# Optimization experiments

Hardware: AMD Instinct MI355X
Metric: run time of the kernel (lower is better)

## Reference

```python
import jax, jax.numpy as jnp
import numpy as np

V, D, H, HD, L, T, B = 65, 384, 6, 64, 6, 256, 64
EPS = 1e-3  # keras LayerNormalization default epsilon


def setup_inputs() -> dict:
    key = jax.random.key(0)
    ks = jax.random.split(key, 12)
    s = 0.02
    n = lambda k, shp: jax.random.normal(k, shp, dtype=jnp.float32) * s
    return {
        "idx": jax.random.randint(ks[0], (B, T), 0, V),
        "tok_emb": n(ks[1], (V, D)),
        "pos_emb": n(ks[2], (T, D)),
        "Wq": n(ks[3], (L, H, D, HD)),
        "Wk": n(ks[4], (L, H, D, HD)),
        "Wv": n(ks[5], (L, H, D, HD)),
        "Wproj": n(ks[6], (L, D, D)),
        "bproj": jnp.zeros((L, D), jnp.float32),
        "W1": n(ks[7], (L, D, 4 * D)),
        "b1": jnp.zeros((L, 4 * D), jnp.float32),
        "W2": n(ks[8], (L, 4 * D, D)),
        "b2": jnp.zeros((L, D), jnp.float32),
        "ln1_g": jnp.ones((L, D), jnp.float32),
        "ln1_b": jnp.zeros((L, D), jnp.float32),
        "ln2_g": jnp.ones((L, D), jnp.float32),
        "ln2_b": jnp.zeros((L, D), jnp.float32),
        "lnf_g": jnp.ones((D,), jnp.float32),
        "lnf_b": jnp.zeros((D,), jnp.float32),
        "Whead": n(ks[9], (D, V)),
        "bhead": jnp.zeros((V,), jnp.float32),
    }


def _ln(x, g, b):
    m = jnp.mean(x, axis=-1, keepdims=True)
    v = jnp.mean(jnp.square(x - m), axis=-1, keepdims=True)
    return (x - m) * jax.lax.rsqrt(v + EPS) * g + b


def reference(idx, tok_emb, pos_emb, Wq, Wk, Wv, Wproj, bproj, W1, b1, W2, b2,
              ln1_g, ln1_b, ln2_g, ln2_b, lnf_g, lnf_b, Whead, bhead):
    Bn, Tn = idx.shape
    x = tok_emb[idx] + pos_emb[:Tn]  # [B,T,D]
    mask = jnp.tril(jnp.ones((Tn, Tn), dtype=bool))
    scale = jnp.float32(D) ** -0.5  # NOTE: original scales by full C=n_embd, not head_size
    for l in range(L):
        h = _ln(x, ln1_g[l], ln1_b[l])
        q = jnp.einsum('btd,hdk->bhtk', h, Wq[l])
        k = jnp.einsum('btd,hdk->bhtk', h, Wk[l])
        v = jnp.einsum('btd,hdk->bhtk', h, Wv[l])
        wei = jnp.einsum('bhtk,bhsk->bhts', q, k) * scale
        wei = jnp.where(mask, wei, -jnp.inf)
        wei = jax.nn.softmax(wei, axis=-1)
        att = jnp.einsum('bhts,bhsk->bhtk', wei, v)
        att = att.transpose(0, 2, 1, 3).reshape(Bn, Tn, D)  # concat heads
        x = x + att @ Wproj[l] + bproj[l]
        h2 = _ln(x, ln2_g[l], ln2_b[l])
        x = x + jax.nn.relu(h2 @ W1[l] + b1[l]) @ W2[l] + b2[l]
    x = _ln(x, lnf_g, lnf_b)
    return x @ Whead + bhead  # logits [B,T,V]
```

## Files before the change

### kernel.cpp

```cpp
#include <hip/hip_runtime.h>
#include <hip/hip_bf16.h>

#define B_  64
#define T_  256
#define D_  384
#define H_  6
#define HD_ 64
#define L_  6
#define V_  65
#define BT  (B_*T_)

typedef __hip_bfloat16 bf16;
typedef unsigned short u16;
typedef short s16;
typedef __attribute__((ext_vector_type(8))) short bf16x8;
typedef __attribute__((ext_vector_type(4))) float f32x4;

#define OFF_QKV   0
#define OFF_PROJ  442368
#define OFF_W1T   589824
#define OFF_W2T   1179648
#define OFF_BPROJ 1769472
#define OFF_B1    1769856
#define OFF_B2    1771392
#define OFF_LN1G  1771776
#define OFF_LN1B  1772160
#define OFF_LN2G  1772544
#define OFF_LN2B  1772928
#define WBUF_E    1773312
#define HOFF_WHT  0
#define HOFF_BH   24960
#define HOFF_LNFG 25088
#define HOFF_LNFB 25472
#define HBUF_E    25856

__device__ __forceinline__ float u2f(u16 u) {
  union { unsigned i; float f; } c; c.i = ((unsigned)u) << 16; return c.f;
}
__device__ __forceinline__ bf16 f2b(float x) { return __float2bfloat16(x); }
__device__ __forceinline__ float b2f(bf16 x) { return __bfloat162float(x); }
__device__ __forceinline__ u16 f2u(float x) { bf16 h = f2b(x); return *(u16*)&h; }

__device__ __forceinline__ float pload(const void* p, size_t i, bool f32w) {
  return f32w ? ((const float*)p)[i] : u2f(((const u16*)p)[i]);
}

__device__ __forceinline__ void swz(int gid, int ntc, int mtiles,
                                    int& nt, int& mblk) {
  if ((mtiles & 7) == 0) {
    int per = ntc << 3;
    int g   = gid / per;
    int rem = gid - g * per;
    nt   = rem >> 3;
    mblk = (g << 3) + (rem & 7);
  } else {
    nt   = gid / mtiles;
    mblk = gid - nt * mtiles;
  }
}

__global__ __launch_bounds__(256) void detect_kernel(
    const void* p1,  const void* p2,  const void* p3,  const void* p4,
    const void* p5,  const void* p6,  const void* p7,  const void* p8,
    const void* p9,  const void* p10, const void* p11, const void* p12,
    const void* p13, const void* p14, const void* p15, const void* p16,
    const void* p17, const void* p18, const void* p19,
    const int* __restrict__ idx, unsigned* flags)
{
  const void* ps[20] = {nullptr, p1, p2, p3, p4, p5, p6, p7, p8, p9, p10,
                        p11, p12, p13, p14, p15, p16, p17, p18, p19};
  const int esz[20] = {16384, 24960, 98304, 884736, 884736, 884736, 884736,
                       2304, 3538944, 9216, 3538944, 2304, 2304, 2304, 2304,
                       2304, 384, 384, 24960, 65};
  __shared__ int r1[256], r2[256];
  int bid = blockIdx.x, tid = threadIdx.x;
  if (bid == 19) {
    int z = 0;
    for (int m = tid; m < 4096; m += 256) z += (idx[2 * m + 1] == 0) ? 1 : 0;
    r1[tid] = z; __syncthreads();
    for (int s = 128; s > 0; s >>= 1) {
      if (tid < s) r1[tid] += r1[tid + s];
      __syncthreads();
    }
    if (tid == 0) flags[20] = (r1[0] >= 4000) ? 1u : 0u;
    return;
  }
  int j = bid + 1;
  const u16* p = (const u16*)ps[j];
  int ns = esz[j] / 2; if (ns > 1024) ns = 1024;
  int band = 0, nz = 0;
  for (int i = tid; i < ns; i += 256) {
    u16 lo = p[2 * i], hi = p[2 * i + 1];
    int e = (lo >> 7) & 0xFF;
    band += (e >= 100 && e <= 127) ? 1 : 0;
    nz   += (lo | hi) ? 1 : 0;
  }
  r1[tid] = band; r2[tid] = nz; __syncthreads();
  for (int s = 128; s > 0; s >>= 1) {
    if (tid < s) { r1[tid] += r1[tid + s]; r2[tid] += r2[tid + s]; }
    __syncthreads();
  }
  if (tid == 0) flags[j] = (r2[0] > 0 && r1[0] * 2 < ns) ? 1u : 0u;
}

__global__ void const_kernel(float* out, int n, float val) {
  int i = blockIdx.x * 256 + threadIdx.x;
  if (i < n) out[i] = val;
}

__device__ __forceinline__ float conv_val(int e, int l,
    const void* Wq, const void* Wk, const void* Wv, const void* Wproj,
    const void* bproj, const void* W1, const void* b1, const void* W2,
    const void* b2, const void* ln1g, const void* ln1b, const void* ln2g,
    const void* ln2b, const unsigned* __restrict__ flags)
{
  float v;
  if (e < OFF_PROJ) {
    int math = e / 24576;
    int rem  = e - math * 24576;
    int hd = rem / 384, d = rem - hd * 384;
    int mat = math / 6, hh = math - mat * 6;
    const void* src = (mat == 0 ? Wq : mat == 1 ? Wk : Wv);
    v = pload(src, ((size_t)(l * 6 + hh) * 384 + d) * 64 + hd, flags[3 + mat] != 0);
  } else if (e < OFF_W1T) {
    int e2 = e - OFF_PROJ;
    int n = e2 / 384, d = e2 - n * 384;
    v = pload(Wproj, ((size_t)l * 384 + d) * 384 + n, flags[6] != 0);
  } else if (e < OFF_W2T) {
    int e2 = e - OFF_W1T;
    int n = e2 / 384, d = e2 - n * 384;
    v = pload(W1, ((size_t)l * 384 + d) * 1536 + n, flags[8] != 0);
  } else if (e < OFF_BPROJ) {
    int e2 = e - OFF_W2T;
    int n = e2 / 1536, k = e2 - n * 1536;
    v = pload(W2, ((size_t)l * 1536 + k) * 384 + n, flags[10] != 0);
  } else {
    int e2 = e - OFF_BPROJ;
    if      (e2 < 384)  v = pload(bproj, (size_t)l * 384 + e2, flags[7] != 0);
    else if (e2 < 1920) v = pload(b1, (size_t)l * 1536 + (e2 - 384), flags[9] != 0);
    else if (e2 < 2304) v = pload(b2, (size_t)l * 384 + (e2 - 1920), flags[11] != 0);
    else if (e2 < 2688) v = pload(ln1g, (size_t)l * 384 + (e2 - 2304), flags[12] != 0);
    else if (e2 < 3072) v = pload(ln1b, (size_t)l * 384 + (e2 - 2688), flags[13] != 0);
    else if (e2 < 3456) v = pload(ln2g, (size_t)l * 384 + (e2 - 3072), flags[14] != 0);
    else                v = pload(ln2b, (size_t)l * 384 + (e2 - 3456), flags[15] != 0);
  }
  return v;
}

__global__ __launch_bounds__(256) void conv_layer(
    const void* Wq, const void* Wk, const void* Wv, const void* Wproj,
    const void* bproj, const void* W1, const void* b1, const void* W2,
    const void* b2, const void* ln1g, const void* ln1b, const void* ln2g,
    const void* ln2b, const unsigned* __restrict__ flags,
    bf16* __restrict__ dst, int l)
{
  int e = blockIdx.x * 256 + threadIdx.x;
  if (e >= WBUF_E) return;
  dst[e] = f2b(conv_val(e, l, Wq, Wk, Wv, Wproj, bproj, W1, b1, W2, b2,
                        ln1g, ln1b, ln2g, ln2b, flags));
}

__global__ __launch_bounds__(256) void convT(
    const void* Wq, const void* Wk, const void* Wv, const void* Wproj,
    const void* W1, const void* W2,
    const unsigned* __restrict__ flags, bf16* __restrict__ dst)
{
  __shared__ float lds[64][65];
  int g = blockIdx.x;
  int l = g / 432, t = g - l * 432;
  const void* sp; bool f32w;
  size_t s_base; int s_rstride;
  size_t d_base; int d_rstride;
  if (t < 108) {
    int mh = t / 6, dt = t - mh * 6;
    int mat = mh / 6;
    sp = (mat == 0 ? Wq : mat == 1 ? Wk : Wv);
    f32w = flags[3 + mat] != 0;
    s_base = ((size_t)l * 6 * 384 + (size_t)(mh - mat * 6) * 384 + dt * 64) * 64;
    s_rstride = 64;
    d_base = (size_t)OFF_QKV + (size_t)mh * 24576 + dt * 64;
    d_rstride = 384;
  } else if (t < 144) {
    int u = t - 108; int nt = u / 6, dt = u - nt * 6;
    sp = Wproj; f32w = flags[6] != 0;
    s_base = ((size_t)l * 384 + dt * 64) * 384 + nt * 64;
    s_rstride = 384;
    d_base = (size_t)OFF_PROJ + (size_t)nt * 64 * 384 + dt * 64;
    d_rstride = 384;
  } else if (t < 288) {
    int u = t - 144; int nt = u / 6, dt = u - nt * 6;
    sp = W1; f32w = flags[8] != 0;
    s_base = ((size_t)l * 384 + dt * 64) * 1536 + nt * 64;
    s_rstride = 1536;
    d_base = (size_t)OFF_W1T + (size_t)nt * 64 * 384 + dt * 64;
    d_rstride = 384;
  } else {
    int u = t - 288; int kt = u / 6, nt = u - kt * 6;
    sp = W2; f32w = flags[10] != 0;
    s_base = ((size_t)l * 1536 + kt * 64) * 384 + nt * 64;
    s_rstride = 384;
    d_base = (size_t)OFF_W2T + (size_t)nt * 64 * 1536 + kt * 64;
    d_rstride = 1536;
  }
  int tid = threadIdx.x;
  int rq = tid >> 6, c = tid & 63;
#pragma unroll
  for (int p = 0; p < 16; p++) {
    int r = p * 4 + rq;
    lds[c][r] = pload(sp, s_base + (size_t)r * s_rstride + c, f32w);
  }
  __syncthreads();
  bf16* dp = dst + (size_t)l * WBUF_E + d_base;
#pragma unroll
  for (int p = 0; p < 16; p++) {
    int cc = p * 4 + rq;
    dp[(size_t)cc * d_rstride + c] = f2b(lds[cc][c]);
  }
}

__global__ __launch_bounds__(256) void convsmall(
    const void* Wq, const void* Wk, const void* Wv, const void* Wproj,
    const void* bproj, const void* W1, const void* b1, const void* W2,
    const void* b2, const void* ln1g, const void* ln1b, const void* ln2g,
    const void* ln2b, const unsigned* __restrict__ flags,
    bf16* __restrict__ dst)
{
  int g = blockIdx.x * 256 + threadIdx.x;
  if (g >= 6 * (WBUF_E - OFF_BPROJ)) return;
  int l = g / (WBUF_E - OFF_BPROJ);
  int e = OFF_BPROJ + (g - l * (WBUF_E - OFF_BPROJ));
  dst[(size_t)l * WBUF_E + e] =
      f2b(conv_val(e, l, Wq, Wk, Wv, Wproj, bproj, W1, b1, W2, b2,
                   ln1g, ln1b, ln2g, ln2b, flags));
}

__global__ __launch_bounds__(256) void conv_head(
    const void* Wh, const void* bh, const void* lnfg, const void* lnfb,
    const unsigned* __restrict__ flags, bf16* __restrict__ dst)
{
  int e = blockIdx.x * 256 + threadIdx.x;
  if (e >= HBUF_E) return;
  float v = 0.f;
  if (e < HOFF_BH) {
    int n = e / 384, d = e - n * 384;
    v = pload(Wh, (size_t)d * 65 + n, flags[18] != 0);
  } else if (e < 25025) {
    v = pload(bh, e - HOFF_BH, flags[19] != 0);
  } else if (e < HOFF_LNFG) {
    v = 0.f;
  } else if (e < HOFF_LNFB) {
    v = pload(lnfg, e - HOFF_LNFG, flags[16] != 0);
  } else {
    v = pload(lnfb, e - HOFF_LNFB, flags[17] != 0);
  }
  dst[e] = f2b(v);
}

__global__ __launch_bounds__(256) void embed_kernel(
    const void* __restrict__ idx, const void* __restrict__ tok,
    const void* __restrict__ pos, bf16* __restrict__ x,
    const unsigned* __restrict__ flags)
{
  int i   = blockIdx.x * 256 + threadIdx.x;
  int tkn = i / D_;
  int d   = i - tkn * D_;
  int t   = tkn & (T_ - 1);
  long long tix;
  if (flags[20]) tix = ((const long long*)idx)[tkn];
  else           tix = ((const int*)idx)[tkn];
  float v = pload(tok, (size_t)tix * D_ + d, flags[1] != 0)
          + pload(pos, (size_t)t * D_ + d, flags[2] != 0);
  x[i] = f2b(v);
}

__global__ __launch_bounds__(256) void lnw_kernel(
    const bf16* __restrict__ x, const u16* __restrict__ g,
    const u16* __restrict__ b, bf16* __restrict__ hc, int tok0)
{
  int w = threadIdx.x >> 6, lane = threadIdx.x & 63;
  int lm = blockIdx.x * 4 + w;
  const u16* xr = (const u16*)x + (size_t)(tok0 + lm) * D_;
  float v[6]; float s = 0.f;
#pragma unroll
  for (int j = 0; j < 3; j++) {
    unsigned pk = *(const unsigned*)(xr + 2 * lane + 128 * j);
    v[2 * j]     = u2f((u16)(pk & 0xFFFF));
    v[2 * j + 1] = u2f((u16)(pk >> 16));
    s += v[2 * j] + v[2 * j + 1];
  }
#pragma unroll
  for (int o = 1; o < 64; o <<= 1) s += __shfl_xor(s, o, 64);
  float mean = s * (1.0f / D_);
  float sq = 0.f;
#pragma unroll
  for (int j = 0; j < 6; j++) { float d0 = v[j] - mean; sq += d0 * d0; }
#pragma unroll
  for (int o = 1; o < 64; o <<= 1) sq += __shfl_xor(sq, o, 64);
  float inv = 1.0f / sqrtf(sq * (1.0f / D_) + 1e-3f);
  u16* hr = (u16*)hc + (size_t)lm * D_;
#pragma unroll
  for (int j = 0; j < 3; j++) {
    int d = 2 * lane + 128 * j;
    unsigned gg = *(const unsigned*)(g + d);
    unsigned bb = *(const unsigned*)(b + d);
    u16 o0 = f2u((v[2 * j]     - mean) * inv * u2f((u16)(gg & 0xFFFF)) + u2f((u16)(bb & 0xFFFF)));
    u16 o1 = f2u((v[2 * j + 1] - mean) * inv * u2f((u16)(gg >> 16))    + u2f((u16)(bb >> 16)));
    *(unsigned*)(hr + d) = ((unsigned)o1 << 16) | o0;
  }
}

__device__ __forceinline__ void gll16(const void* g, void* l) {
  __builtin_amdgcn_global_load_lds(
      (const __attribute__((address_space(1))) unsigned*)g,
      (__attribute__((address_space(3))) unsigned*)l, 16, 0, 0);
}

__device__ __forceinline__ bf16x8 ldfrag(const s16* lds, int r, int s) {
  return *(const bf16x8*)(lds + r * 64 + ((s ^ (r & 7)) << 3));
}

template<int NT, class Epi>
__device__ __forceinline__ void mcore(
    s16* __restrict__ As, s16* __restrict__ Wl,
    const u16* __restrict__ A, const u16* __restrict__ WT,
    int N, int K, int arow0, int n0, Epi epi)
{
  constexpr int MREP = (NT == 128) ? 4 : 2;
  constexpr int WPW  = NT / 32;
  int tid = threadIdx.x;
  int w = tid >> 6, lane = tid & 63;
  int quad = lane >> 4, l15 = lane & 15;
  int r8 = lane >> 3;
  int sl = ((lane & 7) ^ r8) * 8;
  int wm = (NT == 128) ? ((w >> 1) * 64) : (w * 32);
  int wn = (NT == 128) ? ((w & 1) * 64) : 0;

  f32x4 acc[MREP][4];
#pragma unroll
  for (int i = 0; i < MREP; i++)
#pragma unroll
    for (int j = 0; j < 4; j++) acc[i][j] = (f32x4){0.f, 0.f, 0.f, 0.f};

  const u16* Ag[4];
#pragma unroll
  for (int i = 0; i < 4; i++)
    Ag[i] = A + (size_t)(arow0 + (w * 4 + i) * 8 + r8) * K + sl;
  const u16* Wg[WPW];
#pragma unroll
  for (int i = 0; i < WPW; i++)
    Wg[i] = WT + (size_t)(n0 + (w * WPW + i) * 8 + r8) * K + sl;

  for (int k0 = 0; k0 < K; k0 += 64) {
    __syncthreads();
#pragma unroll
    for (int i = 0; i < 4; i++)
      gll16(Ag[i] + k0, As + (w * 4 + i) * 512);
#pragma unroll
    for (int i = 0; i < WPW; i++)
      gll16(Wg[i] + k0, Wl + (w * WPW + i) * 512);
    __syncthreads();
#pragma unroll
    for (int kh = 0; kh < 2; kh++) {
      bf16x8 am[MREP], bn[4];
#pragma unroll
      for (int i = 0; i < MREP; i++)
        am[i] = ldfrag(As, wm + i * 16 + l15, kh * 4 + quad);
#pragma unroll
      for (int j = 0; j < 4; j++)
        bn[j] = ldfrag(Wl, wn + j * 16 + l15, kh * 4 + quad);
#pragma unroll
      for (int i = 0; i < MREP; i++)
#pragma unroll
        for (int j = 0; j < 4; j++)
          acc[i][j] = __builtin_amdgcn_mfma_f32_16x16x32_bf16(am[i], bn[j], acc[i][j], 0, 0, 0);
    }
  }

#pragma unroll
  for (int i = 0; i < MREP; i++)
#pragma unroll
    for (int j = 0; j < 4; j++)
#pragma unroll
      for (int r = 0; r < 4; r++) {
        int m = wm + i * 16 + quad * 4 + r;
        int n = n0 + wn + j * 16 + l15;
        if (n < N) epi(m, n, acc[i][j][r]);
      }
}

__global__ __launch_bounds__(256) void qkv128(
    const bf16* hc, const bf16* Wbuf, bf16* qkvc, int MCa, int mtiles)
{
  __shared__ __attribute__((aligned(16))) s16 As[128 * 64];
  __shared__ __attribute__((aligned(16))) s16 Ws[128 * 64];
  int nt, mblk;
  swz(blockIdx.x, 9, mtiles, nt, mblk);
  int n0 = nt * 128, mloc0 = mblk * 128;
  auto epi = [&](int m, int n, float v) {
    int mat = n / 384;
    int rem = n - mat * 384;
    int hh = rem >> 6, hd = rem & 63;
    qkvc[(size_t)mat * MCa * D_ + (size_t)hh * MCa * HD_
         + (size_t)(mloc0 + m) * HD_ + hd] = f2b(v);
  };
  mcore<128>(As, Ws, (const u16*)hc,
             (const u16*)Wbuf + OFF_QKV, 1152, D_, mloc0, n0, epi);
}

__global__ __launch_bounds__(256) void ffn1_128(
    const bf16* hc, const bf16* Wbuf, bf16* midc, int mtiles)
{
  __shared__ __attribute__((aligned(16))) s16 As[128 * 64];
  __shared__ __attribute__((aligned(16))) s16 Ws[128 * 64];
  int nt, mblk;
  swz(blockIdx.x, 12, mtiles, nt, mblk);
  int n0 = nt * 128, m0 = mblk * 128;
  const bf16* bias = (const bf16*)Wbuf + OFF_B1;
  auto epi = [&](int m, int n, float v) {
    float r = v + b2f(bias[n]);
    midc[(size_t)(m0 + m) * (4 * D_) + n] = f2b(fmaxf(r, 0.f));
  };
  mcore<128>(As, Ws, (const u16*)hc,
             (const u16*)Wbuf + OFF_W1T, 4 * D_, D_, m0, n0, epi);
}

__global__ __launch_bounds__(256) void proj_mfma(
    const bf16* A, const bf16* Wbuf, bf16* x, int tok0, int mtiles)
{
  __shared__ __attribute__((aligned(16))) s16 As[128 * 64];
  __shared__ __attribute__((aligned(16))) s16 Ws[64 * 64];
  int nt, mblk;
  swz(blockIdx.x, 6, mtiles, nt, mblk);
  int n0 = nt * 64, m0 = mblk * 128;
  const bf16* bias = (const bf16*)Wbuf + OFF_BPROJ;
  auto epi = [&](int m, int n, float v) {
    size_t o = (size_t)(tok0 + m0 + m) * D_ + n;
    x[o] = f2b(v + b2f(bias[n]) + b2f(x[o]));
  };
  mcore<64>(As, Ws, (const u16*)A,
            (const u16*)Wbuf + OFF_PROJ, D_, D_, m0, n0, epi);
}

__global__ __launch_bounds__(256) void ffn2_mfma(
    const bf16* midc, const bf16* Wbuf, bf16* x, int tok0, int mtiles)
{
  __shared__ __attribute__((aligned(16))) s16 As[128 * 64];
  __shared__ __attribute__((aligned(16))) s16 Ws[64 * 64];
  int nt, mblk;
  swz(blockIdx.x, 6, mtiles, nt, mblk);
  int n0 = nt * 64, m0 = mblk * 128;
  const bf16* bias = (const bf16*)Wbuf + OFF_B2;
  auto epi = [&](int m, int n, float v) {
    size_t o = (size_t)(tok0 + m0 + m) * D_ + n;
    x[o] = f2b(v + b2f(bias[n]) + b2f(x[o]));
  };
  mcore<64>(As, Ws, (const u16*)midc,
            (const u16*)Wbuf + OFF_W2T, D_, 4 * D_, m0, n0, epi);
}

__global__ __launch_bounds__(256) void head_mfma(
    const bf16* hc, const bf16* Hbuf, float* out, int tok0)
{
  __shared__ __attribute__((aligned(16))) s16 As[128 * 64];
  __shared__ __attribute__((aligned(16))) s16 Ws[64 * 64];
  int n0 = blockIdx.x * 64, m0 = blockIdx.y * 128;
  const bf16* bias = (const bf16*)Hbuf + HOFF_BH;
  auto epi = [&](int m, int n, float v) {
    out[(size_t)(tok0 + m0 + m) * V_ + n] = v + b2f(bias[n]);
  };
  mcore<64>(As, Ws, (const u16*)hc,
            (const u16*)Hbuf + HOFF_WHT, V_, D_, m0, n0, epi);
}

__global__ __launch_bounds__(256) void attn4_kernel(
    const bf16* __restrict__ Q, const bf16* __restrict__ K,
    const bf16* __restrict__ V, bf16* __restrict__ att, int MCa)
{
  __shared__ s16 Qs[64 * 72];
  __shared__ s16 Ks[64 * 72];
  __shared__ __attribute__((aligned(16))) s16 Vt[64 * 64];
  __shared__ s16 Ps[4][16 * 72];
  const float scale = 0.05103103630798288f;
  int tid = threadIdx.x;
  int w = tid >> 6, lane = tid & 63;
  int quad = lane >> 4, l15 = lane & 15;
  int bid = blockIdx.x;
  int qt = bid & 3;
  int bh = bid >> 2;
  int b = bh / H_, h = bh - b * H_;
  size_t base = ((size_t)h * MCa + (size_t)b * T_) * HD_;
  int q0 = qt * 64;
  int cq = qt;

  int rstg = (tid & 7) + 8 * (tid >> 6);
  int sstg = (tid >> 3) & 7;

#pragma unroll
  for (int i = 0; i < 2; i++) {
    int r = rstg + 32 * i;
    *(bf16x8*)&Qs[r * 72 + sstg * 8] =
        *(const bf16x8*)((const u16*)Q + base + (size_t)(q0 + r) * HD_ + sstg * 8);
  }

  float mrow[4] = {-1e30f, -1e30f, -1e30f, -1e30f};
  float lrow[4] = {0.f, 0.f, 0.f, 0.f};
  f32x4 O[4];
#pragma unroll
  for (int nt = 0; nt < 4; nt++) O[nt] = (f32x4){0.f, 0.f, 0.f, 0.f};

  for (int c = 0; c <= cq; c++) {
    __syncthreads();
#pragma unroll
    for (int i = 0; i < 2; i++) {
      int r = rstg + 32 * i;
      *(bf16x8*)&Ks[r * 72 + sstg * 8] =
          *(const bf16x8*)((const u16*)K + base + (size_t)(c * 64 + r) * HD_ + sstg * 8);
      bf16x8 vv =
          *(const bf16x8*)((const u16*)V + base + (size_t)(c * 64 + r) * HD_ + sstg * 8);
      int rs = r >> 3, rl = r & 7;
      int so = ((rs ^ sstg) << 3) + rl;
#pragma unroll
      for (int k = 0; k < 8; k++)
        Vt[(sstg * 8 + k) * 64 + so] = vv[k];
    }
    __syncthreads();

    f32x4 S[4];
#pragma unroll
    for (int nt = 0; nt < 4; nt++) S[nt] = (f32x4){0.f, 0.f, 0.f, 0.f};
#pragma unroll
    for (int ks = 0; ks < 2; ks++) {
      int kk = ks * 32 + quad * 8;
      bf16x8 a = *(const bf16x8*)&Qs[(w * 16 + l15) * 72 + kk];
#pragma unroll
      for (int nt = 0; nt < 4; nt++) {
        bf16x8 bb8 = *(const bf16x8*)&Ks[(nt * 16 + l15) * 72 + kk];
        S[nt] = __builtin_amdgcn_mfma_f32_16x16x32_bf16(a, bb8, S[nt], 0, 0, 0);
      }
    }

#pragma unroll
    for (int nt = 0; nt < 4; nt++)
#pragma unroll
      for (int r = 0; r < 4; r++) {
        int qrow = q0 + w * 16 + quad * 4 + r;
        int sg = c * 64 + nt * 16 + l15;
        float v = S[nt][r] * scale;
        S[nt][r] = (sg <= qrow) ? v : -1e30f;
      }

    float alpha[4];
#pragma unroll
    for (int r = 0; r < 4; r++) {
      float mc = fmaxf(fmaxf(S[0][r], S[1][r]), fmaxf(S[2][r], S[3][r]));
#pragma unroll
      for (int o = 1; o < 16; o <<= 1) mc = fmaxf(mc, __shfl_xor(mc, o, 64));
      float mn = fmaxf(mrow[r], mc);
      alpha[r] = __expf(mrow[r] - mn);
      mrow[r] = mn;
      float s = 0.f;
#pragma unroll
      for (int nt = 0; nt < 4; nt++) {
        float p = __expf(S[nt][r] - mn);
        S[nt][r] = p;
        s += p;
      }
#pragma unroll
      for (int o = 1; o < 16; o <<= 1) s += __shfl_xor(s, o, 64);
      lrow[r] = lrow[r] * alpha[r] + s;
    }
#pragma unroll
    for (int nt = 0; nt < 4; nt++)
#pragma unroll
      for (int r = 0; r < 4; r++) O[nt][r] *= alpha[r];

#pragma unroll
    for (int nt = 0; nt < 4; nt++)
#pragma unroll
      for (int r = 0; r < 4; r++)
        Ps[w][(quad * 4 + r) * 72 + nt * 16 + l15] = (s16)f2u(S[nt][r]);
    __syncthreads();
#pragma unroll
    for (int ks = 0; ks < 2; ks++) {
      bf16x8 a = *(const bf16x8*)&Ps[w][l15 * 72 + ks * 32 + quad * 8];
#pragma unroll
      for (int nt = 0; nt < 4; nt++) {
        int d = nt * 16 + l15;
        bf16x8 bb8 = *(const bf16x8*)&Vt[d * 64 +
            (((ks * 4 + quad) ^ ((d >> 3) & 7)) << 3)];
        O[nt] = __builtin_amdgcn_mfma_f32_16x16x32_bf16(a, bb8, O[nt], 0, 0, 0);
      }
    }
  }

#pragma unroll
  for (int r = 0; r < 4; r++) {
    float invl = 1.0f / lrow[r];
#pragma unroll
    for (int nt = 0; nt < 4; nt++) {
      int qrow = q0 + w * 16 + quad * 4 + r;
      att[(size_t)(b * T_ + qrow) * D_ + h * HD_ + nt * 16 + l15] =
          f2b(O[nt][r] * invl);
    }
  }
}

extern "C" void kernel_launch(void* const* d_in, const int* in_sizes, int n_in,
                              void* d_out, int out_size, void* d_ws, size_t ws_size,
                              hipStream_t stream)
{
  float* out = (float*)d_out;
  dim3 blk(256);
  int outg = (out_size + 255) / 256;

  static const int expected[20] = {
      16384, 24960, 98304, 884736, 884736, 884736, 884736, 2304,
      3538944, 9216, 3538944, 2304, 2304, 2304, 2304, 2304, 384, 384,
      24960, 65};
  if (n_in != 20) { const_kernel<<<outg, blk, 0, stream>>>(out, out_size, 5.0f); return; }
  for (int i = 0; i < 20; i++)
    if (in_sizes[i] != expected[i]) {
      const_kernel<<<outg, blk, 0, stream>>>(out, out_size, 10.0f * (i + 1));
      return;
    }
  if (out_size != BT * V_) { const_kernel<<<outg, blk, 0, stream>>>(out, out_size, 7.0f); return; }

  const void* idx   = d_in[0];
  const void* tok   = d_in[1];
  const void* pos   = d_in[2];
  const void* Wq    = d_in[3];
  const void* Wk    = d_in[4];
  const void* Wv    = d_in[5];
  const void* Wproj = d_in[6];
  const void* bproj = d_in[7];
  const void* W1    = d_in[8];
  const void* b1    = d_in[9];
  const void* W2    = d_in[10];
  const void* b2    = d_in[11];
  const void* ln1g  = d_in[12];
  const void* ln1b  = d_in[13];
  const void* ln2g  = d_in[14];
  const void* ln2b  = d_in[15];
  const void* lnfg  = d_in[16];
  const void* lnfb  = d_in[17];
  const void* Whead = d_in[18];
  const void* bhead = d_in[19];

  const size_t off_x  = 256;
  const size_t off_wb = off_x + (size_t)BT * D_ * 2;
  int nl = 6;
  size_t off_hb = off_wb + (size_t)nl * WBUF_E * 2;
  size_t fixed  = off_hb + ((size_t)HBUF_E * 2 + 63) / 64 * 64;
  size_t minchunk = (size_t)5 * (BT / 64) * D_ * 2;
  if (ws_size < fixed + minchunk) {
    nl = 1;
    off_hb = off_wb + (size_t)WBUF_E * 2;
    fixed  = off_hb + ((size_t)HBUF_E * 2 + 63) / 64 * 64;
  }
  if (ws_size < fixed) {
    const_kernel<<<outg, blk, 0, stream>>>(out, out_size, 0.0f);
    return;
  }
  size_t region = ws_size - fixed;

  int nc = 0;
  const int candn[7] = {1, 2, 4, 8, 16, 32, 64};
  for (int i = 0; i < 7; i++)
    if ((size_t)5 * (BT / candn[i]) * D_ * 2 <= region) { nc = candn[i]; break; }
  if (!nc) { const_kernel<<<outg, blk, 0, stream>>>(out, out_size, 0.0f); return; }
  const int MCc = BT / nc;
  const int CBc = MCc / T_;
  const int mtiles = MCc / 128;

  char* wsb = (char*)d_ws;
  unsigned* flags = (unsigned*)wsb;
  bf16*   x    = (bf16*)(wsb + off_x);
  bf16*   Wbuf = (bf16*)(wsb + off_wb);
  bf16*   Hbuf = (bf16*)(wsb + off_hb);
  bf16*   hc   = (bf16*)(wsb + fixed);
  bf16*   qkvc = hc + (size_t)MCc * D_;
  bf16*   attc = qkvc + (size_t)3 * MCc * D_;
  bf16*   midc = qkvc;

  detect_kernel<<<dim3(20), blk, 0, stream>>>(
      tok, pos, Wq, Wk, Wv, Wproj, bproj, W1, b1, W2, b2,
      ln1g, ln1b, ln2g, ln2b, lnfg, lnfb, Whead, bhead,
      (const int*)idx, flags);
  embed_kernel<<<dim3(BT * D_ / 256), blk, 0, stream>>>(idx, tok, pos, x, flags);
  conv_head<<<dim3((HBUF_E + 255) / 256), blk, 0, stream>>>(
      Whead, bhead, lnfg, lnfb, flags, Hbuf);
  if (nl == 6) {
    convT<<<dim3(6 * 432), blk, 0, stream>>>(
        Wq, Wk, Wv, Wproj, W1, W2, flags, Wbuf);
    convsmall<<<dim3((6 * (WBUF_E - OFF_BPROJ) + 255) / 256), blk, 0, stream>>>(
        Wq, Wk, Wv, Wproj, bproj, W1, b1, W2, b2,
        ln1g, ln1b, ln2g, ln2b, flags, Wbuf);
  }

  for (int l = 0; l < L_; l++) {
    const bf16* Wl = Wbuf + (nl == 6 ? (size_t)l * WBUF_E : 0);
    if (nl == 1)
      conv_layer<<<dim3((WBUF_E + 255) / 256), blk, 0, stream>>>(
          Wq, Wk, Wv, Wproj, bproj, W1, b1, W2, b2,
          ln1g, ln1b, ln2g, ln2b, flags, Wbuf, l);
    for (int c = 0; c < nc; c++) {
      int tok0 = c * MCc;
      lnw_kernel<<<dim3(MCc / 4), blk, 0, stream>>>(
          x, (const u16*)Wl + OFF_LN1G, (const u16*)Wl + OFF_LN1B, hc, tok0);
      qkv128<<<dim3(9 * mtiles), blk, 0, stream>>>(hc, Wl, qkvc, MCc, mtiles);
      attn4_kernel<<<dim3(CBc * H_ * 4), blk, 0, stream>>>(
          qkvc, qkvc + (size_t)MCc * D_, qkvc + (size_t)2 * MCc * D_, attc, MCc);
      proj_mfma<<<dim3(6 * mtiles), blk, 0, stream>>>(attc, Wl, x, tok0, mtiles);
    }
    for (int f = 0; f < nc; f++) {
      int tok0 = f * MCc;
      lnw_kernel<<<dim3(MCc / 4), blk, 0, stream>>>(
          x, (const u16*)Wl + OFF_LN2G, (const u16*)Wl + OFF_LN2B, hc, tok0);
      ffn1_128<<<dim3(12 * mtiles), blk, 0, stream>>>(hc, Wl, midc, mtiles);
      ffn2_mfma<<<dim3(6 * mtiles), blk, 0, stream>>>(midc, Wl, x, tok0, mtiles);
    }
  }

  for (int c = 0; c < nc; c++) {
    int tok0 = c * MCc;
    lnw_kernel<<<dim3(MCc / 4), blk, 0, stream>>>(
        x, (const u16*)Hbuf + HOFF_LNFG, (const u16*)Hbuf + HOFF_LNFB, hc, tok0);
    head_mfma<<<dim3(2, MCc / 128), blk, 0, stream>>>(hc, Hbuf, out, tok0);
  }
}
```

Before: 1.043 ms.

## Double-buffer GEMM LDS tiles with async prefetch and one barrier per step

Rewrites the shared MFMA GEMM core to use two LDS buffers of K-depth 32 instead of one of depth 64. The global-to-LDS loads for the next K step are issued before computing on the current buffer, so load latency can overlap with the MFMAs, and each iteration needs only one barrier. This also drops the XOR swizzle on LDS fragment reads, which may bring back bank conflicts. It doubles the number of K iterations and relies on the barrier waiting for the async LDS loads to finish.

```diff
diff --git a/kernel.cpp b/kernel.cpp
--- a/kernel.cpp
+++ b/kernel.cpp
@@ -315,10 +315,6 @@
       (__attribute__((address_space(3))) unsigned*)l, 16, 0, 0);
 }
 
-__device__ __forceinline__ bf16x8 ldfrag(const s16* lds, int r, int s) {
-  return *(const bf16x8*)(lds + r * 64 + ((s ^ (r & 7)) << 3));
-}
-
 template<int NT, class Epi>
 __device__ __forceinline__ void mcore(
     s16* __restrict__ As, s16* __restrict__ Wl,
@@ -326,12 +322,14 @@
     int N, int K, int arow0, int n0, Epi epi)
 {
   constexpr int MREP = (NT == 128) ? 4 : 2;
-  constexpr int WPW  = NT / 32;
+  constexpr int WPW  = NT / 64;
+  constexpr int ABUF = 128 * 32;
+  constexpr int WBUF = NT * 32;
   int tid = threadIdx.x;
   int w = tid >> 6, lane = tid & 63;
   int quad = lane >> 4, l15 = lane & 15;
-  int r8 = lane >> 3;
-  int sl = ((lane & 7) ^ r8) * 8;
+  int r16 = lane >> 2;
+  int kc  = (lane & 3) * 8;
   int wm = (NT == 128) ? ((w >> 1) * 64) : (w * 32);
   int wn = (NT == 128) ? ((w & 1) * 64) : 0;
 
@@ -341,39 +339,48 @@
 #pragma unroll
     for (int j = 0; j < 4; j++) acc[i][j] = (f32x4){0.f, 0.f, 0.f, 0.f};
 
-  const u16* Ag[4];
-#pragma unroll
-  for (int i = 0; i < 4; i++)
-    Ag[i] = A + (size_t)(arow0 + (w * 4 + i) * 8 + r8) * K + sl;
+  const u16* Ag[2];
+#pragma unroll
+  for (int i = 0; i < 2; i++)
+    Ag[i] = A + (size_t)(arow0 + (w * 2 + i) * 16 + r16) * K + kc;
   const u16* Wg[WPW];
 #pragma unroll
   for (int i = 0; i < WPW; i++)
-    Wg[i] = WT + (size_t)(n0 + (w * WPW + i) * 8 + r8) * K + sl;
-
-  for (int k0 = 0; k0 < K; k0 += 64) {
+    Wg[i] = WT + (size_t)(n0 + (w * WPW + i) * 16 + r16) * K + kc;
+
+  int nk = K >> 5;
+#pragma unroll
+  for (int i = 0; i < 2; i++) gll16(Ag[i], As + (w * 2 + i) * 512);
+#pragma unroll
+  for (int i = 0; i < WPW; i++) gll16(Wg[i], Wl + (w * WPW + i) * 512);
+
+  int cur = 0;
+  for (int t = 0; t < nk; t++) {
     __syncthreads();
-#pragma unroll
-    for (int i = 0; i < 4; i++)
-      gll16(Ag[i] + k0, As + (w * 4 + i) * 512);
-#pragma unroll
-    for (int i = 0; i < WPW; i++)
-      gll16(Wg[i] + k0, Wl + (w * WPW + i) * 512);
-    __syncthreads();
-#pragma unroll
-    for (int kh = 0; kh < 2; kh++) {
-      bf16x8 am[MREP], bn[4];
-#pragma unroll
-      for (int i = 0; i < MREP; i++)
-        am[i] = ldfrag(As, wm + i * 16 + l15, kh * 4 + quad);
+    if (t + 1 < nk) {
+      int k0 = (t + 1) << 5;
+      s16* An = As + (cur ^ 1) * ABUF;
+      s16* Wn = Wl + (cur ^ 1) * WBUF;
+#pragma unroll
+      for (int i = 0; i < 2; i++) gll16(Ag[i] + k0, An + (w * 2 + i) * 512);
+#pragma unroll
+      for (int i = 0; i < WPW; i++) gll16(Wg[i] + k0, Wn + (w * WPW + i) * 512);
+    }
+    const s16* Ab = As + cur * ABUF;
+    const s16* Wb = Wl + cur * WBUF;
+    bf16x8 am[MREP], bn[4];
+#pragma unroll
+    for (int i = 0; i < MREP; i++)
+      am[i] = *(const bf16x8*)(Ab + (wm + i * 16 + l15) * 32 + quad * 8);
+#pragma unroll
+    for (int j = 0; j < 4; j++)
+      bn[j] = *(const bf16x8*)(Wb + (wn + j * 16 + l15) * 32 + quad * 8);
+#pragma unroll
+    for (int i = 0; i < MREP; i++)
 #pragma unroll
       for (int j = 0; j < 4; j++)
-        bn[j] = ldfrag(Wl, wn + j * 16 + l15, kh * 4 + quad);
-#pragma unroll
-      for (int i = 0; i < MREP; i++)
-#pragma unroll
-        for (int j = 0; j < 4; j++)
-          acc[i][j] = __builtin_amdgcn_mfma_f32_16x16x32_bf16(am[i], bn[j], acc[i][j], 0, 0, 0);
-    }
+        acc[i][j] = __builtin_amdgcn_mfma_f32_16x16x32_bf16(am[i], bn[j], acc[i][j], 0, 0, 0);
+    cur ^= 1;
   }
 
 #pragma unroll
@@ -391,8 +398,8 @@
 __global__ __launch_bounds__(256) void qkv128(
     const bf16* hc, const bf16* Wbuf, bf16* qkvc, int MCa, int mtiles)
 {
-  __shared__ __attribute__((aligned(16))) s16 As[128 * 64];
-  __shared__ __attribute__((aligned(16))) s16 Ws[128 * 64];
+  __shared__ __attribute__((aligned(16))) s16 As[2 * 128 * 32];
+  __shared__ __attribute__((aligned(16))) s16 Ws[2 * 128 * 32];
   int nt, mblk;
   swz(blockIdx.x, 9, mtiles, nt, mblk);
   int n0 = nt * 128, mloc0 = mblk * 128;
@@ -410,8 +417,8 @@
 __global__ __launch_bounds__(256) void ffn1_128(
     const bf16* hc, const bf16* Wbuf, bf16* midc, int mtiles)
 {
-  __shared__ __attribute__((aligned(16))) s16 As[128 * 64];
-  __shared__ __attribute__((aligned(16))) s16 Ws[128 * 64];
+  __shared__ __attribute__((aligned(16))) s16 As[2 * 128 * 32];
+  __shared__ __attribute__((aligned(16))) s16 Ws[2 * 128 * 32];
   int nt, mblk;
   swz(blockIdx.x, 12, mtiles, nt, mblk);
   int n0 = nt * 128, m0 = mblk * 128;
@@ -427,8 +434,8 @@
 __global__ __launch_bounds__(256) void proj_mfma(
     const bf16* A, const bf16* Wbuf, bf16* x, int tok0, int mtiles)
 {
-  __shared__ __attribute__((aligned(16))) s16 As[128 * 64];
-  __shared__ __attribute__((aligned(16))) s16 Ws[64 * 64];
+  __shared__ __attribute__((aligned(16))) s16 As[2 * 128 * 32];
+  __shared__ __attribute__((aligned(16))) s16 Ws[2 * 64 * 32];
   int nt, mblk;
   swz(blockIdx.x, 6, mtiles, nt, mblk);
   int n0 = nt * 64, m0 = mblk * 128;
@@ -444,8 +451,8 @@
 __global__ __launch_bounds__(256) void ffn2_mfma(
     const bf16* midc, const bf16* Wbuf, bf16* x, int tok0, int mtiles)
 {
-  __shared__ __attribute__((aligned(16))) s16 As[128 * 64];
-  __shared__ __attribute__((aligned(16))) s16 Ws[64 * 64];
+  __shared__ __attribute__((aligned(16))) s16 As[2 * 128 * 32];
+  __shared__ __attribute__((aligned(16))) s16 Ws[2 * 64 * 32];
   int nt, mblk;
   swz(blockIdx.x, 6, mtiles, nt, mblk);
   int n0 = nt * 64, m0 = mblk * 128;
@@ -461,8 +468,8 @@
 __global__ __launch_bounds__(256) void head_mfma(
     const bf16* hc, const bf16* Hbuf, float* out, int tok0)
 {
-  __shared__ __attribute__((aligned(16))) s16 As[128 * 64];
-  __shared__ __attribute__((aligned(16))) s16 Ws[64 * 64];
+  __shared__ __attribute__((aligned(16))) s16 As[2 * 128 * 32];
+  __shared__ __attribute__((aligned(16))) s16 Ws[2 * 64 * 32];
   int n0 = blockIdx.x * 64, m0 = blockIdx.y * 128;
   const bf16* bias = (const bf16*)Hbuf + HOFF_BH;
   auto epi = [&](int m, int n, float v) {
```

Result: slower. 1.214 ms (+16.4%).
